# Performance work log

Hardware: AMD Instinct MI355X
Metric: run time of the kernel (lower is better)

## Reference

```python
import jax, jax.numpy as jnp
import numpy as np

H, C = 8, 32  # heads, out_channels
NEG_SLOPE = 0.2


def setup_inputs() -> dict:
    key = jax.random.key(0)
    k1, k2, k3, k4, k5 = jax.random.split(key, 5)
    N, IN, E, NNZ = 50000, 256, 10000, 320000
    X = jax.random.normal(k1, (N, IN), dtype=jnp.float32)
    # Linear(in, H*C, bias=False): weight [H*C, IN], scaled like kaiming-uniform-ish
    W = jax.random.normal(k2, (H * C, IN), dtype=jnp.float32) * (1.0 / np.sqrt(IN))
    # glorot init for att_e [1, H, C]
    stdv = np.sqrt(6.0 / (H + C))
    att_e = jax.random.uniform(k3, (1, H, C), dtype=jnp.float32, minval=-stdv, maxval=stdv)
    vertex = jax.random.randint(k4, (NNZ,), 0, N, dtype=jnp.int64)
    edges = jax.random.randint(k5, (NNZ,), 0, E, dtype=jnp.int64)
    return {"X": X, "W": W, "att_e": att_e, "vertex": vertex, "edges": edges, "num_edges": E}


def reference(X, W, att_e, vertex, edges, num_edges):
    N = X.shape[0]
    X0 = X @ W.T                                   # [N, H*C]
    Xh = X0.reshape(N, H, C)                       # [N, H, C]
    Xve = Xh[vertex]                               # [nnz, H, C] gather
    # scatter-mean over hyperedges (first_aggregate='mean')
    Xe_sum = jax.ops.segment_sum(Xve, edges, num_segments=num_edges)
    cnt = jax.ops.segment_sum(jnp.ones(vertex.shape, X.dtype), edges, num_segments=num_edges)
    Xe = Xe_sum / jnp.maximum(cnt, 1.0)[:, None, None]   # [E, H, C]
    alpha_e = (Xe * att_e).sum(-1)                 # [E, H]
    a_ev = alpha_e[edges]                          # [nnz, H]
    a = jax.nn.leaky_relu(a_ev, NEG_SLOPE)
    # segment softmax grouped by destination vertex
    amax = jax.ops.segment_max(a, vertex, num_segments=N)
    amax = jnp.where(jnp.isfinite(amax), amax, 0.0)
    ex = jnp.exp(a - amax[vertex])
    denom = jax.ops.segment_sum(ex, vertex, num_segments=N)
    alpha = ex / (denom[vertex] + 1e-16)           # [nnz, H]
    # attn-weighted scatter-sum back to vertices (dropout p=0.0 -> identity)
    Xev = Xe[edges] * alpha[:, :, None]            # [nnz, H, C]
    Xv = jax.ops.segment_sum(Xev, vertex, num_segments=N)  # [N, H, C]
    Xout = Xv.reshape(N, H * C)
    # use_norm: l2 row-normalize with detached norm
    norm = jax.lax.stop_gradient(jnp.linalg.norm(Xout, axis=1, keepdims=True))
    scale = jnp.where(norm > 0, 1.0 / norm, 0.0)
    return Xout * scale
```

## Files before the change

kernel.cpp:

```cpp
#include <hip/hip_runtime.h>
#include <cmath>

#define HC 256
#define H_ 8
#define C_ 32
#define E_CONST 10000
#define CAPE 160
#define CAPV 32
#define CSTRIDE 16
#define NEG_SLOPE 0.2f

typedef __attribute__((ext_vector_type(8))) short short8;
typedef __attribute__((ext_vector_type(4))) short short4v;
typedef __attribute__((ext_vector_type(4))) float f32x4;

static __device__ inline unsigned short f2bf(float f) {
    unsigned u = __float_as_uint(f);
    unsigned r = u + 0x7FFFu + ((u >> 16) & 1u);
    return (unsigned short)(r >> 16);
}
static __device__ inline float bf2f(unsigned short s) {
    return __uint_as_float(((unsigned)s) << 16);
}
static __device__ inline float bflo(unsigned u) { return __uint_as_float(u << 16); }
static __device__ inline float bfhi(unsigned u) { return __uint_as_float(u & 0xffff0000u); }
static __device__ inline unsigned pk2bf(float lo, float hi) {
    return (unsigned)f2bf(lo) | ((unsigned)f2bf(hi) << 16);
}

#define GLD16(gp, lp) __builtin_amdgcn_global_load_lds( \
    (const __attribute__((address_space(1))) unsigned int*)(gp), \
    (__attribute__((address_space(3))) unsigned int*)(lp), 16, 0, 0)

static __device__ inline void rowfma(float* A, uint4 xv, float p) {
    A[0] += p * bflo(xv.x); A[1] += p * bfhi(xv.x);
    A[2] += p * bflo(xv.y); A[3] += p * bfhi(xv.y);
    A[4] += p * bflo(xv.z); A[5] += p * bfhi(xv.z);
    A[6] += p * bflo(xv.w); A[7] += p * bfhi(xv.w);
}

static __device__ inline void fill_bucket16(
        const int* __restrict__ vertex, const int* __restrict__ edges,
        int* cnt, unsigned short* bucket, int nnz, int base,
        bool key_is_edge, int cap) {
    int i0 = base + threadIdx.x * 16;
    int vv[16], ee[16];
    if (i0 + 16 <= nnz) {
        const int4* vp = (const int4*)(vertex + i0);
        const int4* ep = (const int4*)(edges + i0);
        #pragma unroll
        for (int q = 0; q < 4; ++q) {
            int4 a = vp[q], b = ep[q];
            vv[q * 4 + 0] = a.x; vv[q * 4 + 1] = a.y;
            vv[q * 4 + 2] = a.z; vv[q * 4 + 3] = a.w;
            ee[q * 4 + 0] = b.x; ee[q * 4 + 1] = b.y;
            ee[q * 4 + 2] = b.z; ee[q * 4 + 3] = b.w;
        }
        #pragma unroll
        for (int k = 0; k < 16; ++k) {
            int key = key_is_edge ? ee[k] : vv[k];
            int val = key_is_edge ? vv[k] : ee[k];
            int p = atomicAdd(&cnt[key * CSTRIDE], 1);
            if (p < cap) bucket[(size_t)key * cap + p] = (unsigned short)val;
        }
    } else {
        for (int k = 0; k < 16; ++k) {
            int i = i0 + k;
            if (i < nnz) {
                int v = vertex[i], e = edges[i];
                int key = key_is_edge ? e : v;
                int val = key_is_edge ? v : e;
                int p = atomicAdd(&cnt[key * CSTRIDE], 1);
                if (p < cap) bucket[(size_t)key * cap + p] = (unsigned short)val;
            }
        }
    }
}

__global__ __launch_bounds__(256) void k_pre(
        const float* __restrict__ X, const float* __restrict__ W,
        const float* __restrict__ att,
        unsigned short* __restrict__ Xb, unsigned short* __restrict__ Wb,
        float* __restrict__ w_att, int nX, int nW, int fillB,
        const int* __restrict__ vertex, const int* __restrict__ edges,
        int* cnt_e, unsigned short* bucket_e, int nnz) {
    const int bid = blockIdx.x;
    const int t   = threadIdx.x;
    if (bid == 0) {
        float acc[H_] = {};
        for (int c = 0; c < C_; ++c) {
            #pragma unroll
            for (int h = 0; h < H_; ++h)
                acc[h] += W[(size_t)(h * C_ + c) * 256 + t] * att[h * C_ + c];
        }
        #pragma unroll
        for (int h = 0; h < H_; ++h) w_att[h * 256 + t] = acc[h];
        return;
    }
    if (bid <= fillB) {
        fill_bucket16(vertex, edges, cnt_e, bucket_e, nnz,
                      (bid - 1) * 4096, true, CAPE);
        return;
    }
    int g = (bid - 1 - fillB) * 256 + t;
    int nXg = nX >> 3;
    int nTg = (nX + nW) >> 3;
    if (g >= nTg) return;
    const float* src;
    unsigned short* dst;
    int base;
    if (g < nXg) { src = X; dst = Xb; base = g << 3; }
    else         { src = W; dst = Wb; base = (g - nXg) << 3; }
    float4 a = *(const float4*)(src + base);
    float4 b = *(const float4*)(src + base + 4);
    uint4 o;
    o.x = pk2bf(a.x, a.y);
    o.y = pk2bf(a.z, a.w);
    o.z = pk2bf(b.x, b.y);
    o.w = pk2bf(b.z, b.w);
    *(uint4*)(dst + base) = o;
}

__global__ __launch_bounds__(256) void k_edge_mean(
        const unsigned short* __restrict__ Xb,
        const float* __restrict__ w_att,
        const int* __restrict__ cnt_e,
        const unsigned short* __restrict__ bucket_e,
        unsigned short* __restrict__ Xm,
        float* __restrict__ alpha_e, int E, int fillVB,
        const int* __restrict__ vertex, const int* __restrict__ edges,
        int* cnt_v, unsigned short* bucket_v, int nnz) {
    if ((int)blockIdx.x < fillVB) {
        fill_bucket16(vertex, edges, cnt_v, bucket_v, nnz,
                      blockIdx.x * 4096, false, CAPV);
        return;
    }
    int wid = ((blockIdx.x - fillVB) * blockDim.x + threadIdx.x) >> 6;
    int l    = threadIdx.x & 63;
    int half = l >> 5;
    int lh   = l & 31;
    int e = wid * 2 + half;
    if (e >= E) return;
    int m = cnt_e[e * CSTRIDE];
    if (m > CAPE) m = CAPE;
    const unsigned short* be = bucket_e + (size_t)e * CAPE;
    const unsigned short* xbase = Xb + 8 * lh;
    float acc0[8] = {}, acc1[8] = {};
    int j = 0;
    for (; j + 16 <= m; j += 16) {
        uint4 ia = *(const uint4*)(be + j);
        uint4 ib = *(const uint4*)(be + j + 8);
        unsigned w[8] = {ia.x, ia.y, ia.z, ia.w, ib.x, ib.y, ib.z, ib.w};
        uint4 xs[16];
        #pragma unroll
        for (int k = 0; k < 8; ++k) {
            xs[2 * k]     = *(const uint4*)(xbase + (size_t)(w[k] & 0xffff) * 256);
            xs[2 * k + 1] = *(const uint4*)(xbase + (size_t)(w[k] >> 16) * 256);
        }
        #pragma unroll
        for (int k = 0; k < 16; k += 2) {
            rowfma(acc0, xs[k], 1.0f);
            rowfma(acc1, xs[k + 1], 1.0f);
        }
    }
    for (; j + 8 <= m; j += 8) {
        uint4 idv = *(const uint4*)(be + j);
        unsigned w[4] = {idv.x, idv.y, idv.z, idv.w};
        uint4 xs[8];
        #pragma unroll
        for (int k = 0; k < 4; ++k) {
            xs[2 * k]     = *(const uint4*)(xbase + (size_t)(w[k] & 0xffff) * 256);
            xs[2 * k + 1] = *(const uint4*)(xbase + (size_t)(w[k] >> 16) * 256);
        }
        #pragma unroll
        for (int k = 0; k < 8; k += 2) {
            rowfma(acc0, xs[k], 1.0f);
            rowfma(acc1, xs[k + 1], 1.0f);
        }
    }
    for (; j + 4 <= m; j += 4) {
        int v0 = be[j], v1 = be[j + 1], v2 = be[j + 2], v3 = be[j + 3];
        uint4 x0 = *(const uint4*)(xbase + (size_t)v0 * 256);
        uint4 x1 = *(const uint4*)(xbase + (size_t)v1 * 256);
        uint4 x2 = *(const uint4*)(xbase + (size_t)v2 * 256);
        uint4 x3 = *(const uint4*)(xbase + (size_t)v3 * 256);
        rowfma(acc0, x0, 1.0f); rowfma(acc1, x1, 1.0f);
        rowfma(acc0, x2, 1.0f); rowfma(acc1, x3, 1.0f);
    }
    for (; j < m; ++j) {
        int v0 = be[j];
        uint4 x0 = *(const uint4*)(xbase + (size_t)v0 * 256);
        rowfma(acc0, x0, 1.0f);
    }
    float inv = 1.0f / (float)(m > 1 ? m : 1);
    float mean[8];
    #pragma unroll
    for (int c = 0; c < 8; ++c) mean[c] = (acc0[c] + acc1[c]) * inv;
    uint4 o;
    o.x = pk2bf(mean[0], mean[1]);
    o.y = pk2bf(mean[2], mean[3]);
    o.z = pk2bf(mean[4], mean[5]);
    o.w = pk2bf(mean[6], mean[7]);
    *(uint4*)(Xm + (size_t)e * 256 + 8 * lh) = o;
    float s[H_];
    #pragma unroll
    for (int h = 0; h < H_; ++h) {
        const float4* wv = (const float4*)(w_att + h * 256 + 8 * lh);
        float4 w0 = wv[0], w1 = wv[1];
        s[h] = mean[0] * w0.x + mean[1] * w0.y + mean[2] * w0.z + mean[3] * w0.w
             + mean[4] * w1.x + mean[5] * w1.y + mean[6] * w1.z + mean[7] * w1.w;
    }
    #pragma unroll
    for (int off = 1; off < 32; off <<= 1)
        #pragma unroll
        for (int h = 0; h < H_; ++h) s[h] += __shfl_xor(s[h], off, 64);
    if (lh == 0) {
        float4 a0, a1;
        float* ap0 = (float*)&a0; float* ap1 = (float*)&a1;
        #pragma unroll
        for (int h = 0; h < 4; ++h) {
            float av = s[h] > 0.f ? s[h] : NEG_SLOPE * s[h];
            ap0[h] = av;
        }
        #pragma unroll
        for (int h = 4; h < 8; ++h) {
            float av = s[h] > 0.f ? s[h] : NEG_SLOPE * s[h];
            ap1[h - 4] = av;
        }
        float4* dst = (float4*)(alpha_e + (size_t)e * H_);
        dst[0] = a0; dst[1] = a1;
    }
}

__global__ __launch_bounds__(256) void k_gemm(const unsigned short* __restrict__ Ain,
                                              const unsigned short* __restrict__ Bin,
                                              unsigned short* __restrict__ Cout,
                                              int Nrows, int nbx) {
    __shared__ unsigned short As[128 * 64];
    __shared__ unsigned short Bs[128 * 64];
    const int t    = threadIdx.x;
    const int lane = t & 63;
    const int wave = t >> 6;
    const int wr   = wave >> 1;
    const int wc   = wave & 1;
    const int bx   = blockIdx.x % nbx;
    const int by   = blockIdx.x / nbx;
    const int r0   = bx * 128;
    const int c0   = by * 128;
    const int ln15 = lane & 15;
    const int q8   = (lane >> 4) * 8;
    const int rw   = lane >> 3;
    const int cf   = (lane & 7) ^ rw;

    f32x4 acc[4][4];
    #pragma unroll
    for (int i = 0; i < 4; ++i)
        #pragma unroll
        for (int j = 0; j < 4; ++j) acc[i][j] = (f32x4){0.f, 0.f, 0.f, 0.f};

    for (int k0 = 0; k0 < 256; k0 += 64) {
        #pragma unroll
        for (int u = 0; u < 4; ++u) {
            int j   = u * 4 + wave;
            int row = j * 8 + rw;
            int gr  = r0 + row;
            if (gr < Nrows)
                GLD16(Ain + (size_t)gr * 256 + k0 + cf * 8, &As[j * 512]);
            GLD16(Bin + (size_t)(c0 + row) * 256 + k0 + cf * 8, &Bs[j * 512]);
        }
        __syncthreads();
        #pragma unroll
        for (int ks = 0; ks < 64; ks += 32) {
            int c = (ks + q8) >> 3;
            short8 af[4], bfr[4];
            #pragma unroll
            for (int mi = 0; mi < 4; ++mi) {
                int mm  = wr * 64 + mi * 16 + ln15;
                int pos = c ^ (mm & 7);
                af[mi] = *(const short8*)(&As[mm * 64 + pos * 8]);
            }
            #pragma unroll
            for (int nj = 0; nj < 4; ++nj) {
                int nn  = wc * 64 + nj * 16 + ln15;
                int pos = c ^ (nn & 7);
                bfr[nj] = *(const short8*)(&Bs[nn * 64 + pos * 8]);
            }
            #pragma unroll
            for (int mi = 0; mi < 4; ++mi)
                #pragma unroll
                for (int nj = 0; nj < 4; ++nj)
                    acc[mi][nj] = __builtin_amdgcn_mfma_f32_16x16x32_bf16(
                        af[mi], bfr[nj], acc[mi][nj], 0, 0, 0);
        }
        __syncthreads();
    }
    const int rowq = (lane >> 4) * 4;
    #pragma unroll
    for (int mi = 0; mi < 4; ++mi) {
        #pragma unroll
        for (int r = 0; r < 4; ++r) {
            int mm = r0 + wr * 64 + mi * 16 + rowq + r;
            if (mm < Nrows) {
                unsigned short* dst = Cout + (size_t)mm * 256 + c0 + wc * 64 + ln15;
                #pragma unroll
                for (int nj = 0; nj < 4; ++nj) dst[nj * 16] = f2bf(acc[mi][nj][r]);
            }
        }
    }
}

__global__ __launch_bounds__(256) void k_vertex_agg(
        const unsigned short* __restrict__ Xe,
        const float* __restrict__ alpha_e,
        const int* __restrict__ cnt_v,
        const unsigned short* __restrict__ bucket_v,
        float* __restrict__ out, int N) {
    int wid  = (blockIdx.x * blockDim.x + threadIdx.x) >> 6;
    int l    = threadIdx.x & 63;
    int half = l >> 5;
    int lh   = l & 31;
    int v = wid * 2 + half;
    if (v >= N) return;
    int mraw = cnt_v[v * CSTRIDE];
    const unsigned short* bv = bucket_v + (size_t)v * CAPV;
    int jl = lh >> 3;
    int hp = lh & 7;
    int h2 = lh >> 2;
    float aload[8];
    #pragma unroll
    for (int b = 0; b < 8; ++b) {
        int jj = b * 4 + jl;
        int ed = bv[jj];
        ed = ed < E_CONST ? ed : 0;
        aload[b] = alpha_e[ed * H_ + hp];
    }
    uint4 xr[8];
    #pragma unroll
    for (int r = 0; r < 8; ++r) {
        int ed = bv[r];
        ed = ed < E_CONST ? ed : 0;
        xr[r] = *(const uint4*)(Xe + (size_t)ed * 256 + 8 * lh);
    }
    int m = mraw > CAPV ? CAPV : mraw;
    float aa[8];
    #pragma unroll
    for (int b = 0; b < 8; ++b) aa[b] = (b * 4 + jl < m) ? aload[b] : -INFINITY;
    float amax = fmaxf(fmaxf(fmaxf(aa[0], aa[1]), fmaxf(aa[2], aa[3])),
                       fmaxf(fmaxf(aa[4], aa[5]), fmaxf(aa[6], aa[7])));
    amax = fmaxf(amax, __shfl_xor(amax, 8, 64));
    amax = fmaxf(amax, __shfl_xor(amax, 16, 64));
    amax = fmaxf(amax, -1e30f);
    float exr[8];
    float dsum = 0.f;
    #pragma unroll
    for (int b = 0; b < 8; ++b) {
        exr[b] = __expf(aa[b] - amax);
        dsum += exr[b];
    }
    dsum += __shfl_xor(dsum, 8, 64);
    dsum += __shfl_xor(dsum, 16, 64);
    float rden = 1.0f / (dsum + 1e-16f);
    #pragma unroll
    for (int b = 0; b < 8; ++b) exr[b] *= rden;
    float accA[8] = {}, accB[8] = {};
    #pragma unroll
    for (int r = 0; r < 8; r += 2) {
        float pA = __shfl(exr[r >> 2], ((r & 3) << 3) | h2, 32);
        float pB = __shfl(exr[(r + 1) >> 2], (((r + 1) & 3) << 3) | h2, 32);
        rowfma(accA, xr[r], pA);
        rowfma(accB, xr[r + 1], pB);
    }
    #pragma unroll
    for (int b = 2; b < 8; ++b) {
        int lo = b * 4;
        if (lo >= m) break;
        int hi = m < lo + 4 ? m : lo + 4;
        #pragma unroll
        for (int jo = 0; jo < 4; ++jo) {
            int j = lo + jo;
            if (j >= hi) break;
            int e0 = bv[j];
            float p = __shfl(exr[b], (jo << 3) | h2, 32);
            uint4 xv = *(const uint4*)(Xe + (size_t)e0 * 256 + 8 * lh);
            if (jo & 1) { rowfma(accB, xv, p); }
            else        { rowfma(accA, xv, p); }
        }
    }
    float acc[8];
    float ss = 0.f;
    #pragma unroll
    for (int c = 0; c < 8; ++c) {
        acc[c] = accA[c] + accB[c];
        ss += acc[c] * acc[c];
    }
    #pragma unroll
    for (int off = 1; off < 32; off <<= 1) ss += __shfl_xor(ss, off, 64);
    float scale = ss > 0.f ? 1.0f / sqrtf(ss) : 0.f;
    float4 o0 = make_float4(acc[0] * scale, acc[1] * scale,
                            acc[2] * scale, acc[3] * scale);
    float4 o1 = make_float4(acc[4] * scale, acc[5] * scale,
                            acc[6] * scale, acc[7] * scale);
    float4* dst = (float4*)(out + (size_t)v * 256 + 8 * lh);
    dst[0] = o0; dst[1] = o1;
}

extern "C" void kernel_launch(void* const* d_in, const int* in_sizes, int n_in,
                              void* d_out, int out_size, void* d_ws, size_t ws_size,
                              hipStream_t stream) {
    const float* X      = (const float*)d_in[0];
    const float* W      = (const float*)d_in[1];
    const float* att    = (const float*)d_in[2];
    const int*   vertex = (const int*)d_in[3];
    const int*   edges  = (const int*)d_in[4];
    const int NNZ = in_sizes[3];
    const int N   = in_sizes[0] / 256;
    const int nX  = in_sizes[0];
    const int nW  = in_sizes[1];
    const int E   = E_CONST;

    char* ws = (char*)d_ws;
    unsigned short* Xb = (unsigned short*)ws; ws += (size_t)nX * 2;
    unsigned short* Wb = (unsigned short*)ws; ws += (size_t)nW * 2;
    unsigned short* Xm = (unsigned short*)ws; ws += (size_t)E * HC * 2;
    unsigned short* Xe = (unsigned short*)ws; ws += (size_t)E * HC * 2;
    float* w_att    = (float*)ws; ws += (size_t)H_ * 256 * 4;
    float* alpha_e  = (float*)ws; ws += (size_t)E * H_ * 4;
    int*   cnt_e    = (int*)ws;   ws += (size_t)E * CSTRIDE * 4;
    int*   cnt_v    = (int*)ws;   ws += (size_t)N * CSTRIDE * 4;
    unsigned short* bucket_e = (unsigned short*)ws; ws += (size_t)E * CAPE * 2;
    unsigned short* bucket_v = (unsigned short*)ws;

    hipMemsetAsync(cnt_e, 0, (size_t)(E + N) * CSTRIDE * 4, stream);

    const int fillB = (NNZ + 4095) / 4096;
    const int cvtB  = (((nX + nW) >> 3) + 255) / 256;
    k_pre<<<1 + fillB + cvtB, 256, 0, stream>>>(
        X, W, att, Xb, Wb, w_att, nX, nW, fillB,
        vertex, edges, cnt_e, bucket_e, NNZ);

    const int fillVB = (NNZ + 4095) / 4096;
    const int eWaves = (E + 1) / 2;
    k_edge_mean<<<fillVB + (eWaves * 64 + 255) / 256, 256, 0, stream>>>(
        Xb, w_att, cnt_e, bucket_e, Xm, alpha_e, E, fillVB,
        vertex, edges, cnt_v, bucket_v, NNZ);

    const int nbx = (E + 127) / 128;
    k_gemm<<<nbx * 2, 256, 0, stream>>>(Xm, Wb, Xe, E, nbx);

    const int vWaves = (N + 1) / 2;
    k_vertex_agg<<<(vWaves * 64 + 255) / 256, 256, 0, stream>>>(
        Xe, alpha_e, cnt_v, bucket_v, (float*)d_out, N);
}
```

Measured before the change: 189.7 us.

## Build edge and vertex buckets in one pass and prefetch more rows in vertex aggregation

The vertex-bucket fill moves out of the edge-mean kernel and into the pre-processing kernel. Each thread now reads its 4 incidence pairs once and does both atomic bucket inserts, and more blocks are launched so there is more parallelism. Separately, vertex aggregation now prefetches 16 unconditional Xe rows instead of 8 to raise memory-level parallelism. The cost is more register pressure, and some extra loads for vertices with fewer than 16 incidences.

```diff
diff --git a/kernel.cpp b/kernel.cpp
--- a/kernel.cpp
+++ b/kernel.cpp
@@ -39,39 +39,33 @@
     A[6] += p * bflo(xv.w); A[7] += p * bfhi(xv.w);
 }
 
-static __device__ inline void fill_bucket16(
+static __device__ inline void fill_both4(
         const int* __restrict__ vertex, const int* __restrict__ edges,
-        int* cnt, unsigned short* bucket, int nnz, int base,
-        bool key_is_edge, int cap) {
-    int i0 = base + threadIdx.x * 16;
-    int vv[16], ee[16];
-    if (i0 + 16 <= nnz) {
-        const int4* vp = (const int4*)(vertex + i0);
-        const int4* ep = (const int4*)(edges + i0);
-        #pragma unroll
-        for (int q = 0; q < 4; ++q) {
-            int4 a = vp[q], b = ep[q];
-            vv[q * 4 + 0] = a.x; vv[q * 4 + 1] = a.y;
-            vv[q * 4 + 2] = a.z; vv[q * 4 + 3] = a.w;
-            ee[q * 4 + 0] = b.x; ee[q * 4 + 1] = b.y;
-            ee[q * 4 + 2] = b.z; ee[q * 4 + 3] = b.w;
-        }
-        #pragma unroll
-        for (int k = 0; k < 16; ++k) {
-            int key = key_is_edge ? ee[k] : vv[k];
-            int val = key_is_edge ? vv[k] : ee[k];
-            int p = atomicAdd(&cnt[key * CSTRIDE], 1);
-            if (p < cap) bucket[(size_t)key * cap + p] = (unsigned short)val;
+        int* cnt_e, unsigned short* bucket_e,
+        int* cnt_v, unsigned short* bucket_v,
+        int nnz, int base) {
+    int i0 = base + threadIdx.x * 4;
+    if (i0 + 4 <= nnz) {
+        int4 a = *(const int4*)(vertex + i0);
+        int4 b = *(const int4*)(edges + i0);
+        int vv[4] = {a.x, a.y, a.z, a.w};
+        int ee[4] = {b.x, b.y, b.z, b.w};
+        #pragma unroll
+        for (int k = 0; k < 4; ++k) {
+            int pe = atomicAdd(&cnt_e[ee[k] * CSTRIDE], 1);
+            int pv = atomicAdd(&cnt_v[vv[k] * CSTRIDE], 1);
+            if (pe < CAPE) bucket_e[(size_t)ee[k] * CAPE + pe] = (unsigned short)vv[k];
+            if (pv < CAPV) bucket_v[(size_t)vv[k] * CAPV + pv] = (unsigned short)ee[k];
         }
     } else {
-        for (int k = 0; k < 16; ++k) {
+        for (int k = 0; k < 4; ++k) {
             int i = i0 + k;
             if (i < nnz) {
                 int v = vertex[i], e = edges[i];
-                int key = key_is_edge ? e : v;
-                int val = key_is_edge ? v : e;
-                int p = atomicAdd(&cnt[key * CSTRIDE], 1);
-                if (p < cap) bucket[(size_t)key * cap + p] = (unsigned short)val;
+                int pe = atomicAdd(&cnt_e[e * CSTRIDE], 1);
+                int pv = atomicAdd(&cnt_v[v * CSTRIDE], 1);
+                if (pe < CAPE) bucket_e[(size_t)e * CAPE + pe] = (unsigned short)v;
+                if (pv < CAPV) bucket_v[(size_t)v * CAPV + pv] = (unsigned short)e;
             }
         }
     }
@@ -83,7 +77,8 @@
         unsigned short* __restrict__ Xb, unsigned short* __restrict__ Wb,
         float* __restrict__ w_att, int nX, int nW, int fillB,
         const int* __restrict__ vertex, const int* __restrict__ edges,
-        int* cnt_e, unsigned short* bucket_e, int nnz) {
+        int* cnt_e, unsigned short* bucket_e,
+        int* cnt_v, unsigned short* bucket_v, int nnz) {
     const int bid = blockIdx.x;
     const int t   = threadIdx.x;
     if (bid == 0) {
@@ -98,8 +93,8 @@
         return;
     }
     if (bid <= fillB) {
-        fill_bucket16(vertex, edges, cnt_e, bucket_e, nnz,
-                      (bid - 1) * 4096, true, CAPE);
+        fill_both4(vertex, edges, cnt_e, bucket_e, cnt_v, bucket_v,
+                   nnz, (bid - 1) * 1024);
         return;
     }
     int g = (bid - 1 - fillB) * 256 + t;
@@ -127,15 +122,8 @@
         const int* __restrict__ cnt_e,
         const unsigned short* __restrict__ bucket_e,
         unsigned short* __restrict__ Xm,
-        float* __restrict__ alpha_e, int E, int fillVB,
-        const int* __restrict__ vertex, const int* __restrict__ edges,
-        int* cnt_v, unsigned short* bucket_v, int nnz) {
-    if ((int)blockIdx.x < fillVB) {
-        fill_bucket16(vertex, edges, cnt_v, bucket_v, nnz,
-                      blockIdx.x * 4096, false, CAPV);
-        return;
-    }
-    int wid = ((blockIdx.x - fillVB) * blockDim.x + threadIdx.x) >> 6;
+        float* __restrict__ alpha_e, int E) {
+    int wid = (blockIdx.x * blockDim.x + threadIdx.x) >> 6;
     int l    = threadIdx.x & 63;
     int half = l >> 5;
     int lh   = l & 31;
@@ -334,9 +322,9 @@
         ed = ed < E_CONST ? ed : 0;
         aload[b] = alpha_e[ed * H_ + hp];
     }
-    uint4 xr[8];
-    #pragma unroll
-    for (int r = 0; r < 8; ++r) {
+    uint4 xr[16];
+    #pragma unroll
+    for (int r = 0; r < 16; ++r) {
         int ed = bv[r];
         ed = ed < E_CONST ? ed : 0;
         xr[r] = *(const uint4*)(Xe + (size_t)ed * 256 + 8 * lh);
@@ -364,14 +352,14 @@
     for (int b = 0; b < 8; ++b) exr[b] *= rden;
     float accA[8] = {}, accB[8] = {};
     #pragma unroll
-    for (int r = 0; r < 8; r += 2) {
+    for (int r = 0; r < 16; r += 2) {
         float pA = __shfl(exr[r >> 2], ((r & 3) << 3) | h2, 32);
         float pB = __shfl(exr[(r + 1) >> 2], (((r + 1) & 3) << 3) | h2, 32);
         rowfma(accA, xr[r], pA);
         rowfma(accB, xr[r + 1], pB);
     }
     #pragma unroll
-    for (int b = 2; b < 8; ++b) {
+    for (int b = 4; b < 8; ++b) {
         int lo = b * 4;
         if (lo >= m) break;
         int hi = m < lo + 4 ? m : lo + 4;
@@ -432,17 +420,15 @@
 
     hipMemsetAsync(cnt_e, 0, (size_t)(E + N) * CSTRIDE * 4, stream);
 
-    const int fillB = (NNZ + 4095) / 4096;
+    const int fillB = (NNZ + 1023) / 1024;
     const int cvtB  = (((nX + nW) >> 3) + 255) / 256;
     k_pre<<<1 + fillB + cvtB, 256, 0, stream>>>(
         X, W, att, Xb, Wb, w_att, nX, nW, fillB,
-        vertex, edges, cnt_e, bucket_e, NNZ);
-
-    const int fillVB = (NNZ + 4095) / 4096;
+        vertex, edges, cnt_e, bucket_e, cnt_v, bucket_v, NNZ);
+
     const int eWaves = (E + 1) / 2;
-    k_edge_mean<<<fillVB + (eWaves * 64 + 255) / 256, 256, 0, stream>>>(
-        Xb, w_att, cnt_e, bucket_e, Xm, alpha_e, E, fillVB,
-        vertex, edges, cnt_v, bucket_v, NNZ);
+    k_edge_mean<<<(eWaves * 64 + 255) / 256, 256, 0, stream>>>(
+        Xb, w_att, cnt_e, bucket_e, Xm, alpha_e, E);
 
     const int nbx = (E + 127) / 128;
     k_gemm<<<nbx * 2, 256, 0, stream>>>(Xm, Wb, Xe, E, nbx);
```

Result: slower. 197.1 us (+3.9%).
